# Kernel optimization log

Measured on AMD Instinct MI355X. Metric: run time of the kernel, lower is better.

The kernel has to match this reference:

```python
import jax, jax.numpy as jnp
import numpy as np

TEMPERATURE = 0.05


def setup_inputs() -> dict:
    key = jax.random.key(0)
    k1, k2, k3 = jax.random.split(key, 3)
    B, D = 8192, 256
    return {
        "embedding_anchor": jax.random.normal(k1, (B, D), dtype=jnp.float32),
        "embedding_pos": jax.random.normal(k2, (B, D), dtype=jnp.float32),
        "embedding_neg": jax.random.normal(k3, (B, D), dtype=jnp.float32),
    }


def _l2norm(x, eps=1e-12):
    # torch.nn.functional.normalize: x / max(||x||, eps)
    n = jnp.sqrt(jnp.sum(x * x, axis=1, keepdims=True))
    return x / jnp.maximum(n, eps)


def reference(embedding_anchor, embedding_pos, embedding_neg):
    B = embedding_anchor.shape[0]
    targets = jnp.concatenate([embedding_pos, embedding_neg], axis=0)  # [2B, D]
    a = _l2norm(embedding_anchor)
    t = _l2norm(targets)
    scores = (a @ t.T) / TEMPERATURE  # [B, 2B]
    # Chunked CE with per-chunk weight len(labels)/B == full-batch mean CE
    logp = jax.nn.log_softmax(scores, axis=1)
    labels = jnp.arange(B)
    loss = -jnp.mean(jnp.take_along_axis(logp, labels[:, None], axis=1))
    return loss
```

## Files before the change

kernel.cpp:

```cpp
#include <hip/hip_runtime.h>
#include <hip/hip_bf16.h>

#define D 256
#define TEMP_INV 20.0f
#define NJ 16
#define NS (NJ * 8)

typedef __attribute__((ext_vector_type(8))) short bf16x8s;
typedef __attribute__((ext_vector_type(4))) float f32x4;

__device__ __forceinline__ unsigned short f2bf(float f) {
  unsigned u = __float_as_uint(f);
  unsigned r = u + 0x7FFFu + ((u >> 16) & 1u);
  return (unsigned short)(r >> 16);
}

__device__ __forceinline__ void gld16(const void* g, void* l) {
  __builtin_amdgcn_global_load_lds(
      (const __attribute__((address_space(1))) void*)g,
      (__attribute__((address_space(3))) void*)l, 16, 0, 0);
}

__global__ __launch_bounds__(256) void nce_normalize(const float* __restrict__ anc,
                                                     const float* __restrict__ pos,
                                                     const float* __restrict__ neg,
                                                     unsigned short* __restrict__ An,
                                                     unsigned short* __restrict__ Tn,
                                                     float* __restrict__ rowsum,
                                                     int B) {
  int zi = blockIdx.x * 256 + threadIdx.x;
  if (blockIdx.x < (B + 255) / 256 && zi < B) rowsum[zi] = 0.0f;

  const int lane = threadIdx.x & 63;
  const int wid  = threadIdx.x >> 6;
  const int sub  = lane >> 4, lr = lane & 15;
  int row = blockIdx.x * 16 + wid * 4 + sub;

  const float* src;
  unsigned short* dst;
  int r2;
  if (row < B)          { src = anc; dst = An; r2 = row; }
  else if (row < 2 * B) { src = pos; dst = Tn; r2 = row - B; }
  else                  { src = neg; dst = Tn + (size_t)B * D; r2 = row - 2 * B; }

  const float4* sp = reinterpret_cast<const float4*>(src) + (size_t)r2 * (D / 4);
  float4 v[4];
#pragma unroll
  for (int c = 0; c < 4; ++c) v[c] = sp[lr + c * 16];
  float ss = 0.0f;
#pragma unroll
  for (int c = 0; c < 4; ++c)
    ss += v[c].x * v[c].x + v[c].y * v[c].y + v[c].z * v[c].z + v[c].w * v[c].w;
  ss += __shfl_xor(ss, 1, 64);
  ss += __shfl_xor(ss, 2, 64);
  ss += __shfl_xor(ss, 4, 64);
  ss += __shfl_xor(ss, 8, 64);
  float inv = rsqrtf(fmaxf(ss, 1e-24f));
  ushort4* dp = reinterpret_cast<ushort4*>(dst) + (size_t)r2 * (D / 4);
#pragma unroll
  for (int c = 0; c < 4; ++c) {
    ushort4 o;
    o.x = f2bf(v[c].x * inv);
    o.y = f2bf(v[c].y * inv);
    o.z = f2bf(v[c].z * inv);
    o.w = f2bf(v[c].w * inv);
    dp[lr + c * 16] = o;
  }
}

__global__ __launch_bounds__(256, 2) void nce_scores(const unsigned short* __restrict__ A,
                                                     const unsigned short* __restrict__ T,
                                                     float* __restrict__ rowsum,
                                                     float* __restrict__ diag) {
  __shared__ unsigned char smem[4][8192];

  const int tid  = threadIdx.x;
  const int lane = tid & 63;
  const int wid  = __builtin_amdgcn_readfirstlane(tid >> 6);
  const int wr = wid >> 1, wc = wid & 1;
  const int row0 = blockIdx.y * 128;
  const int cg   = blockIdx.x;
  const int r = lane & 15, g = lane >> 4;

  const int pp    = (lane & 7) ^ (lane >> 3);
  const int Rbase = 2 * (lane >> 3) + (pp >> 2);
  const int Cb    = pp & 3;
  const unsigned char* gB = (const unsigned char*)T +
      (((size_t)(cg * 2048 + wid * 32 + Rbase)) << 9) + Cb * 16;

  auto STAGE = [&](int s) {
    const unsigned char* gb = gB + (size_t)(s >> 3) * 65536 + (s & 7) * 64;
    unsigned char* sb = &smem[s & 3][0];
    gld16(gb,        sb + wid * 2048);
    gld16(gb + 8192, sb + wid * 2048 + 1024);
  };

  const int S7   = (r >> 1) & 7;
  const int pA   = (((r & 1) << 2) + g) ^ S7;
  const int offF = ((r >> 1) << 7) + (pA << 4);
  const int offB = wc * 4096 + offF;

  const unsigned short* aPtr = A + (size_t)(row0 + wr * 64 + r) * D + g * 8;
  bf16x8s aF[4][8];
#pragma unroll
  for (int m = 0; m < 4; ++m)
#pragma unroll
    for (int kt = 0; kt < 8; ++kt)
      aF[m][kt] = *reinterpret_cast<const bf16x8s*>(aPtr + (size_t)m * 16 * D + kt * 32);

  STAGE(0);
  STAGE(1);
  STAGE(2);

  float rs[4][4];
#pragma unroll
  for (int m = 0; m < 4; ++m)
#pragma unroll
    for (int reg = 0; reg < 4; ++reg) rs[m][reg] = 0.0f;

  for (int j = 0; j < NJ; ++j) {
    f32x4 acc[4][4];
#pragma unroll
    for (int m = 0; m < 4; ++m)
#pragma unroll
      for (int n = 0; n < 4; ++n) acc[m][n] = (f32x4)0.0f;

#pragma unroll
    for (int kt = 0; kt < 8; ++kt) {
      const int s = j * 8 + kt;
      asm volatile("s_waitcnt vmcnt(4)" ::: "memory");
      __builtin_amdgcn_s_barrier();
      const unsigned char* sb = &smem[s & 3][0];
      bf16x8s bF[4];
#pragma unroll
      for (int n = 0; n < 4; ++n)
        bF[n] = *reinterpret_cast<const bf16x8s*>(sb + offB + n * 1024);
      if (s + 3 < NS) STAGE(s + 3);
      asm volatile("s_waitcnt lgkmcnt(0)" ::: "memory");
      __builtin_amdgcn_sched_barrier(0);
      __builtin_amdgcn_s_setprio(1);
#pragma unroll
      for (int m = 0; m < 4; ++m)
#pragma unroll
        for (int n = 0; n < 4; ++n)
          acc[m][n] = __builtin_amdgcn_mfma_f32_16x16x32_bf16(aF[m][kt], bF[n], acc[m][n], 0, 0, 0);
      __builtin_amdgcn_s_setprio(0);
      __builtin_amdgcn_sched_barrier(0);
    }

    const bool diagTile = (cg * NJ + j == (int)blockIdx.y);
#pragma unroll
    for (int m = 0; m < 4; ++m) {
#pragma unroll
      for (int reg = 0; reg < 4; ++reg) {
        float s = 0.0f;
#pragma unroll
        for (int n = 0; n < 4; ++n) s += __expf(acc[m][n][reg] * TEMP_INV);
        rs[m][reg] += s;
        if (diagTile && wr == wc && r == g * 4 + reg)
          diag[row0 + wr * 64 + m * 16 + r] = acc[m][m][reg];
      }
    }
  }

#pragma unroll
  for (int m = 0; m < 4; ++m) {
#pragma unroll
    for (int reg = 0; reg < 4; ++reg) {
      float s = rs[m][reg];
      s += __shfl_xor(s, 1, 64);
      s += __shfl_xor(s, 2, 64);
      s += __shfl_xor(s, 4, 64);
      s += __shfl_xor(s, 8, 64);
      if (r == 0) atomicAdd(&rowsum[row0 + wr * 64 + m * 16 + g * 4 + reg], s);
    }
  }
}

__global__ __launch_bounds__(1024) void nce_finalize(const float* __restrict__ rowsum,
                                                     const float* __restrict__ diag,
                                                     float* __restrict__ out, int n) {
  __shared__ float red[16];
  float s = 0.0f;
  for (int i = threadIdx.x; i < n; i += 1024)
    s += logf(rowsum[i]) - diag[i] * TEMP_INV;
#pragma unroll
  for (int m = 1; m < 64; m <<= 1) s += __shfl_xor(s, m, 64);
  if ((threadIdx.x & 63) == 0) red[threadIdx.x >> 6] = s;
  __syncthreads();
  if (threadIdx.x == 0) {
    float t = 0.0f;
#pragma unroll
    for (int i = 0; i < 16; ++i) t += red[i];
    out[0] = t / (float)n;
  }
}

extern "C" void kernel_launch(void* const* d_in, const int* in_sizes, int n_in,
                              void* d_out, int out_size, void* d_ws, size_t ws_size,
                              hipStream_t stream) {
  const float* anc = (const float*)d_in[0];
  const float* pos = (const float*)d_in[1];
  const float* neg = (const float*)d_in[2];
  const int B  = in_sizes[0] / D;
  const int N2 = 2 * B;

  char* ws = (char*)d_ws;
  unsigned short* An = (unsigned short*)ws;
  unsigned short* Tn = (unsigned short*)(ws + (size_t)B * D * 2);
  float* rowsum = (float*)(ws + (size_t)B * D * 2 + (size_t)N2 * D * 2);
  float* diag   = rowsum + B;

  nce_normalize<<<3 * B / 16, 256, 0, stream>>>(anc, pos, neg, An, Tn, rowsum, B);

  dim3 grid(N2 / (NJ * 128), B / 128);
  nce_scores<<<grid, 256, 0, stream>>>(An, Tn, rowsum, diag);

  nce_finalize<<<1, 1024, 0, stream>>>(rowsum, diag, (float*)d_out, B);
}
```

Baseline: 140.1 us.

## Switch scores GEMM to 32x32x16 MFMA with double-buffered LDS fragment prefetch

Replaces the 16x16x32 bf16 MFMA tiling with 32x32x16 MFMAs, so each wave computes 2x2 tiles of 32x32 and needs fewer LDS fragment loads per FLOP. B fragments for the next k-step are prefetched into a register double buffer while the current MFMAs issue, and the LDS swizzle and staging layout are reworked to match. It also halves NJ, which doubles the grid's column blocks, and raises launch bounds to 4 blocks per CU for more parallelism. In exchange it costs more atomics on rowsum, puts more register pressure on the larger accumulators, and adds risk in the new diagonal and row-index mapping.

New measurement: 298.0 us. +112.8%, slower.

```diff
diff --git a/kernel.cpp b/kernel.cpp
--- a/kernel.cpp
+++ b/kernel.cpp
@@ -3,11 +3,11 @@
 
 #define D 256
 #define TEMP_INV 20.0f
-#define NJ 16
+#define NJ 8
 #define NS (NJ * 8)
 
 typedef __attribute__((ext_vector_type(8))) short bf16x8s;
-typedef __attribute__((ext_vector_type(4))) float f32x4;
+typedef __attribute__((ext_vector_type(16))) float f32x16;
 
 __device__ __forceinline__ unsigned short f2bf(float f) {
   unsigned u = __float_as_uint(f);
@@ -68,7 +68,7 @@
   }
 }
 
-__global__ __launch_bounds__(256, 2) void nce_scores(const unsigned short* __restrict__ A,
+__global__ __launch_bounds__(256, 4) void nce_scores(const unsigned short* __restrict__ A,
                                                      const unsigned short* __restrict__ T,
                                                      float* __restrict__ rowsum,
                                                      float* __restrict__ diag) {
@@ -80,101 +80,131 @@
   const int wr = wid >> 1, wc = wid & 1;
   const int row0 = blockIdx.y * 128;
   const int cg   = blockIdx.x;
-  const int r = lane & 15, g = lane >> 4;
-
-  const int pp    = (lane & 7) ^ (lane >> 3);
-  const int Rbase = 2 * (lane >> 3) + (pp >> 2);
-  const int Cb    = pp & 3;
+  const int r32 = lane & 31, g2 = lane >> 5;
+
+  const int Rl = lane >> 2;
+  const int Cl = (lane & 3) ^ ((lane >> 3) & 3);
   const unsigned char* gB = (const unsigned char*)T +
-      (((size_t)(cg * 2048 + wid * 32 + Rbase)) << 9) + Cb * 16;
-
-  auto STAGE = [&](int s) {
-    const unsigned char* gb = gB + (size_t)(s >> 3) * 65536 + (s & 7) * 64;
-    unsigned char* sb = &smem[s & 3][0];
+      (((size_t)(cg * 1024 + wid * 32 + Rl)) << 9) + Cl * 16;
+
+  auto STAGE = [&](int j2, int kt2, int buf) {
+    const unsigned char* gb = gB + (size_t)j2 * 65536 + kt2 * 64;
+    unsigned char* sb = &smem[buf][0];
     gld16(gb,        sb + wid * 2048);
     gld16(gb + 8192, sb + wid * 2048 + 1024);
   };
 
-  const int S7   = (r >> 1) & 7;
-  const int pA   = (((r & 1) << 2) + g) ^ S7;
-  const int offF = ((r >> 1) << 7) + (pA << 4);
-  const int offB = wc * 4096 + offF;
-
-  const unsigned short* aPtr = A + (size_t)(row0 + wr * 64 + r) * D + g * 8;
-  bf16x8s aF[4][8];
-#pragma unroll
-  for (int m = 0; m < 4; ++m)
-#pragma unroll
-    for (int kt = 0; kt < 8; ++kt)
-      aF[m][kt] = *reinterpret_cast<const bf16x8s*>(aPtr + (size_t)m * 16 * D + kt * 32);
-
-  STAGE(0);
-  STAGE(1);
-  STAGE(2);
-
-  float rs[4][4];
-#pragma unroll
-  for (int m = 0; m < 4; ++m)
-#pragma unroll
-    for (int reg = 0; reg < 4; ++reg) rs[m][reg] = 0.0f;
+  const int xr = (r32 >> 1) & 3;
+  int offB[2][2];
+#pragma unroll
+  for (int s2 = 0; s2 < 2; ++s2)
+#pragma unroll
+    for (int n = 0; n < 2; ++n)
+      offB[s2][n] = ((wc * 64 + n * 32 + r32) << 6) + ((((s2 << 1) | g2) ^ xr) << 4);
+
+  const unsigned short* aPtr = A + (size_t)(row0 + wr * 64 + r32) * D + g2 * 8;
+  bf16x8s aF[2][16];
+#pragma unroll
+  for (int m = 0; m < 2; ++m)
+#pragma unroll
+    for (int ks = 0; ks < 16; ++ks)
+      aF[m][ks] = *reinterpret_cast<const bf16x8s*>(aPtr + (size_t)m * 32 * D + ks * 16);
+
+  float rs[2][16];
+#pragma unroll
+  for (int m = 0; m < 2; ++m)
+#pragma unroll
+    for (int reg = 0; reg < 16; ++reg) rs[m][reg] = 0.0f;
+
+  bf16x8s bF[2][2][2];
+
+  STAGE(0, 0, 0);
+  STAGE(0, 1, 1);
+  STAGE(0, 2, 2);
+  asm volatile("s_waitcnt vmcnt(4)" ::: "memory");
+  __builtin_amdgcn_s_barrier();
+  {
+    const unsigned char* sb0 = &smem[0][0];
+#pragma unroll
+    for (int s2 = 0; s2 < 2; ++s2)
+#pragma unroll
+      for (int n = 0; n < 2; ++n)
+        bF[0][s2][n] = *reinterpret_cast<const bf16x8s*>(sb0 + offB[s2][n]);
+  }
 
   for (int j = 0; j < NJ; ++j) {
-    f32x4 acc[4][4];
-#pragma unroll
-    for (int m = 0; m < 4; ++m)
-#pragma unroll
-      for (int n = 0; n < 4; ++n) acc[m][n] = (f32x4)0.0f;
+    f32x16 acc[2][2];
+#pragma unroll
+    for (int m = 0; m < 2; ++m)
+#pragma unroll
+      for (int n = 0; n < 2; ++n) acc[m][n] = (f32x16)0.0f;
 
 #pragma unroll
     for (int kt = 0; kt < 8; ++kt) {
-      const int s = j * 8 + kt;
-      asm volatile("s_waitcnt vmcnt(4)" ::: "memory");
+      asm volatile("s_waitcnt vmcnt(2)" ::: "memory");
       __builtin_amdgcn_s_barrier();
-      const unsigned char* sb = &smem[s & 3][0];
-      bf16x8s bF[4];
-#pragma unroll
-      for (int n = 0; n < 4; ++n)
-        bF[n] = *reinterpret_cast<const bf16x8s*>(sb + offB + n * 1024);
-      if (s + 3 < NS) STAGE(s + 3);
-      asm volatile("s_waitcnt lgkmcnt(0)" ::: "memory");
+      {
+        const int j2  = j + ((kt + 3) >> 3);
+        const int kt2 = (kt + 3) & 7;
+        if (j2 < NJ) STAGE(j2, kt2, (kt + 3) & 3);
+      }
+      {
+        const unsigned char* sbn = &smem[(kt + 1) & 3][0];
+#pragma unroll
+        for (int s2 = 0; s2 < 2; ++s2)
+#pragma unroll
+          for (int n = 0; n < 2; ++n)
+            bF[(kt + 1) & 1][s2][n] =
+                *reinterpret_cast<const bf16x8s*>(sbn + offB[s2][n]);
+      }
+      asm volatile("s_waitcnt lgkmcnt(4)" ::: "memory");
       __builtin_amdgcn_sched_barrier(0);
       __builtin_amdgcn_s_setprio(1);
 #pragma unroll
-      for (int m = 0; m < 4; ++m)
-#pragma unroll
-        for (int n = 0; n < 4; ++n)
-          acc[m][n] = __builtin_amdgcn_mfma_f32_16x16x32_bf16(aF[m][kt], bF[n], acc[m][n], 0, 0, 0);
+      for (int s2 = 0; s2 < 2; ++s2)
+#pragma unroll
+        for (int m = 0; m < 2; ++m)
+#pragma unroll
+          for (int n = 0; n < 2; ++n)
+            acc[m][n] = __builtin_amdgcn_mfma_f32_32x32x16_bf16(
+                aF[m][kt * 2 + s2], bF[kt & 1][s2][n], acc[m][n], 0, 0, 0);
       __builtin_amdgcn_s_setprio(0);
       __builtin_amdgcn_sched_barrier(0);
     }
 
-    const bool diagTile = (cg * NJ + j == (int)blockIdx.y);
-#pragma unroll
-    for (int m = 0; m < 4; ++m) {
-#pragma unroll
-      for (int reg = 0; reg < 4; ++reg) {
-        float s = 0.0f;
-#pragma unroll
-        for (int n = 0; n < 4; ++n) s += __expf(acc[m][n][reg] * TEMP_INV);
-        rs[m][reg] += s;
-        if (diagTile && wr == wc && r == g * 4 + reg)
-          diag[row0 + wr * 64 + m * 16 + r] = acc[m][m][reg];
-      }
+#pragma unroll
+    for (int m = 0; m < 2; ++m)
+#pragma unroll
+      for (int reg = 0; reg < 16; ++reg)
+        rs[m][reg] += __expf(acc[m][0][reg] * TEMP_INV) +
+                      __expf(acc[m][1][reg] * TEMP_INV);
+
+    const bool diagT = (cg * NJ + j == (int)blockIdx.y);
+    if (diagT && wr == wc) {
+#pragma unroll
+      for (int m = 0; m < 2; ++m)
+#pragma unroll
+        for (int reg = 0; reg < 16; ++reg) {
+          const int crow = (reg & 3) + 8 * (reg >> 2) + 4 * g2;
+          if (r32 == crow)
+            diag[row0 + wr * 64 + m * 32 + crow] = acc[m][m][reg];
+        }
     }
   }
 
 #pragma unroll
-  for (int m = 0; m < 4; ++m) {
-#pragma unroll
-    for (int reg = 0; reg < 4; ++reg) {
+  for (int m = 0; m < 2; ++m)
+#pragma unroll
+    for (int reg = 0; reg < 16; ++reg) {
       float s = rs[m][reg];
       s += __shfl_xor(s, 1, 64);
       s += __shfl_xor(s, 2, 64);
       s += __shfl_xor(s, 4, 64);
       s += __shfl_xor(s, 8, 64);
-      if (r == 0) atomicAdd(&rowsum[row0 + wr * 64 + m * 16 + g * 4 + reg], s);
+      s += __shfl_xor(s, 16, 64);
+      if (r32 == 0)
+        atomicAdd(&rowsum[row0 + wr * 64 + m * 32 + (reg & 3) + 8 * (reg >> 2) + 4 * g2], s);
     }
-  }
 }
 
 __global__ __launch_bounds__(1024) void nce_finalize(const float* __restrict__ rowsum,
```

## Double-buffer LDS B-fragment reads and fuse finalize into scores via last-block counter

Applied to the files above, without the earlier changes.

Prefetches the next k-step's B fragments from LDS into a second register buffer while MFMAs run on the current one, relaxing the vmcnt/lgkmcnt waits. It also removes the separate finalize kernel: each scores block increments a global counter, and the last block computes the log-sum reduction and writes the loss. This cuts LDS-read latency stalls and one kernel launch, at the cost of more registers and a serial tail in one block.

After: 192.3 us. 37.3% more time.

```diff
diff --git a/kernel.cpp b/kernel.cpp
--- a/kernel.cpp
+++ b/kernel.cpp
@@ -27,9 +27,11 @@
                                                      unsigned short* __restrict__ An,
                                                      unsigned short* __restrict__ Tn,
                                                      float* __restrict__ rowsum,
+                                                     int* __restrict__ counter,
                                                      int B) {
   int zi = blockIdx.x * 256 + threadIdx.x;
   if (blockIdx.x < (B + 255) / 256 && zi < B) rowsum[zi] = 0.0f;
+  if (blockIdx.x == 0 && threadIdx.x == 0) *counter = 0;
 
   const int lane = threadIdx.x & 63;
   const int wid  = threadIdx.x >> 6;
@@ -71,8 +73,13 @@
 __global__ __launch_bounds__(256, 2) void nce_scores(const unsigned short* __restrict__ A,
                                                      const unsigned short* __restrict__ T,
                                                      float* __restrict__ rowsum,
-                                                     float* __restrict__ diag) {
+                                                     float* __restrict__ diag,
+                                                     int* __restrict__ counter,
+                                                     float* __restrict__ out,
+                                                     int B, int nblocks) {
   __shared__ unsigned char smem[4][8192];
+  __shared__ float red[4];
+  __shared__ int lastFlag;
 
   const int tid  = threadIdx.x;
   const int lane = tid & 63;
@@ -118,6 +125,17 @@
 #pragma unroll
     for (int reg = 0; reg < 4; ++reg) rs[m][reg] = 0.0f;
 
+  bf16x8s bF[2][4];
+
+  asm volatile("s_waitcnt vmcnt(4)" ::: "memory");
+  __builtin_amdgcn_s_barrier();
+  {
+    const unsigned char* sb0 = &smem[0][0];
+#pragma unroll
+    for (int n = 0; n < 4; ++n)
+      bF[0][n] = *reinterpret_cast<const bf16x8s*>(sb0 + offB + n * 1024);
+  }
+
   for (int j = 0; j < NJ; ++j) {
     f32x4 acc[4][4];
 #pragma unroll
@@ -128,22 +146,24 @@
 #pragma unroll
     for (int kt = 0; kt < 8; ++kt) {
       const int s = j * 8 + kt;
-      asm volatile("s_waitcnt vmcnt(4)" ::: "memory");
+      asm volatile("s_waitcnt vmcnt(2)" ::: "memory");
       __builtin_amdgcn_s_barrier();
-      const unsigned char* sb = &smem[s & 3][0];
-      bf16x8s bF[4];
-#pragma unroll
-      for (int n = 0; n < 4; ++n)
-        bF[n] = *reinterpret_cast<const bf16x8s*>(sb + offB + n * 1024);
       if (s + 3 < NS) STAGE(s + 3);
-      asm volatile("s_waitcnt lgkmcnt(0)" ::: "memory");
+      {
+        const unsigned char* sbn = &smem[(kt + 1) & 3][0];
+#pragma unroll
+        for (int n = 0; n < 4; ++n)
+          bF[(kt + 1) & 1][n] =
+              *reinterpret_cast<const bf16x8s*>(sbn + offB + n * 1024);
+      }
+      asm volatile("s_waitcnt lgkmcnt(4)" ::: "memory");
       __builtin_amdgcn_sched_barrier(0);
       __builtin_amdgcn_s_setprio(1);
 #pragma unroll
       for (int m = 0; m < 4; ++m)
 #pragma unroll
         for (int n = 0; n < 4; ++n)
-          acc[m][n] = __builtin_amdgcn_mfma_f32_16x16x32_bf16(aF[m][kt], bF[n], acc[m][n], 0, 0, 0);
+          acc[m][n] = __builtin_amdgcn_mfma_f32_16x16x32_bf16(aF[m][kt], bF[kt & 1][n], acc[m][n], 0, 0, 0);
       __builtin_amdgcn_s_setprio(0);
       __builtin_amdgcn_sched_barrier(0);
     }
@@ -175,24 +195,20 @@
       if (r == 0) atomicAdd(&rowsum[row0 + wr * 64 + m * 16 + g * 4 + reg], s);
     }
   }
-}
-
-__global__ __launch_bounds__(1024) void nce_finalize(const float* __restrict__ rowsum,
-                                                     const float* __restrict__ diag,
-                                                     float* __restrict__ out, int n) {
-  __shared__ float red[16];
-  float s = 0.0f;
-  for (int i = threadIdx.x; i < n; i += 1024)
-    s += logf(rowsum[i]) - diag[i] * TEMP_INV;
-#pragma unroll
-  for (int m = 1; m < 64; m <<= 1) s += __shfl_xor(s, m, 64);
-  if ((threadIdx.x & 63) == 0) red[threadIdx.x >> 6] = s;
+
+  __threadfence();
+  if (tid == 0) lastFlag = (atomicAdd(counter, 1) == nblocks - 1);
   __syncthreads();
-  if (threadIdx.x == 0) {
-    float t = 0.0f;
-#pragma unroll
-    for (int i = 0; i < 16; ++i) t += red[i];
-    out[0] = t / (float)n;
+  if (lastFlag) {
+    __threadfence();
+    float s = 0.0f;
+    for (int i = tid; i < B; i += 256)
+      s += logf(rowsum[i]) - diag[i] * TEMP_INV;
+#pragma unroll
+    for (int m = 1; m < 64; m <<= 1) s += __shfl_xor(s, m, 64);
+    if ((tid & 63) == 0) red[tid >> 6] = s;
+    __syncthreads();
+    if (tid == 0) out[0] = (red[0] + red[1] + red[2] + red[3]) / (float)B;
   }
 }
 
@@ -210,11 +226,11 @@
   unsigned short* Tn = (unsigned short*)(ws + (size_t)B * D * 2);
   float* rowsum = (float*)(ws + (size_t)B * D * 2 + (size_t)N2 * D * 2);
   float* diag   = rowsum + B;
-
-  nce_normalize<<<3 * B / 16, 256, 0, stream>>>(anc, pos, neg, An, Tn, rowsum, B);
+  int* counter  = (int*)(diag + B);
+
+  nce_normalize<<<3 * B / 16, 256, 0, stream>>>(anc, pos, neg, An, Tn, rowsum, counter, B);
 
   dim3 grid(N2 / (NJ * 128), B / 128);
-  nce_scores<<<grid, 256, 0, stream>>>(An, Tn, rowsum, diag);
-
-  nce_finalize<<<1, 1024, 0, stream>>>(rowsum, diag, (float*)d_out, B);
-}
+  nce_scores<<<grid, 256, 0, stream>>>(An, Tn, rowsum, diag, counter,
+                                       (float*)d_out, B, grid.x * grid.y);
+}
```

## Double K-step per pipeline stage and use raw exp2 in softmax sum

Applied to the files above, without the earlier changes.

Each pipeline stage now loads a 64-wide K slice (16KB per buffer) instead of 32, halving the number of barriers and waits per tile and issuing 32 MFMAs per barrier. The LDS swizzle and load layout are redone for 128-byte rows, with B-fragment offsets precomputed. The exponential uses the hardware exp2 with a folded constant, which avoids the scaling inside __expf. LDS usage doubles to 64KB per block, which may limit occupancy with launch bounds of 2 blocks per CU.

New measurement: 139.2 us. About the same (-0.6%).

```diff
diff --git a/kernel.cpp b/kernel.cpp
--- a/kernel.cpp
+++ b/kernel.cpp
@@ -3,8 +3,9 @@
 
 #define D 256
 #define TEMP_INV 20.0f
+#define K_EXP2 28.85390081777927f
 #define NJ 16
-#define NS (NJ * 8)
+#define NS (NJ * 4)
 
 typedef __attribute__((ext_vector_type(8))) short bf16x8s;
 typedef __attribute__((ext_vector_type(4))) float f32x4;
@@ -72,7 +73,7 @@
                                                      const unsigned short* __restrict__ T,
                                                      float* __restrict__ rowsum,
                                                      float* __restrict__ diag) {
-  __shared__ unsigned char smem[4][8192];
+  __shared__ unsigned char smem[4][16384];
 
   const int tid  = threadIdx.x;
   const int lane = tid & 63;
@@ -82,31 +83,35 @@
   const int cg   = blockIdx.x;
   const int r = lane & 15, g = lane >> 4;
 
-  const int pp    = (lane & 7) ^ (lane >> 3);
-  const int Rbase = 2 * (lane >> 3) + (pp >> 2);
-  const int Cb    = pp & 3;
+  const int Rl = lane >> 3;
+  const int Cl = (lane & 7) ^ Rl;
   const unsigned char* gB = (const unsigned char*)T +
-      (((size_t)(cg * 2048 + wid * 32 + Rbase)) << 9) + Cb * 16;
+      (((size_t)(cg * 2048 + wid * 32 + Rl)) << 9) + Cl * 16;
 
   auto STAGE = [&](int s) {
-    const unsigned char* gb = gB + (size_t)(s >> 3) * 65536 + (s & 7) * 64;
+    const unsigned char* gb = gB + (size_t)(s >> 2) * 65536 + (s & 3) * 128;
     unsigned char* sb = &smem[s & 3][0];
-    gld16(gb,        sb + wid * 2048);
-    gld16(gb + 8192, sb + wid * 2048 + 1024);
+#pragma unroll
+    for (int q = 0; q < 4; ++q)
+      gld16(gb + q * 4096, sb + wid * 4096 + q * 1024);
   };
 
-  const int S7   = (r >> 1) & 7;
-  const int pA   = (((r & 1) << 2) + g) ^ S7;
-  const int offF = ((r >> 1) << 7) + (pA << 4);
-  const int offB = wc * 4096 + offF;
+  const int rx = r & 7;
+  int offB[2][4];
+#pragma unroll
+  for (int ks = 0; ks < 2; ++ks)
+#pragma unroll
+    for (int n = 0; n < 4; ++n)
+      offB[ks][n] = wc * 8192 + n * 2048 + r * 128 + ((((ks << 2) | g) ^ rx) << 4);
 
   const unsigned short* aPtr = A + (size_t)(row0 + wr * 64 + r) * D + g * 8;
   bf16x8s aF[4][8];
 #pragma unroll
   for (int m = 0; m < 4; ++m)
 #pragma unroll
-    for (int kt = 0; kt < 8; ++kt)
-      aF[m][kt] = *reinterpret_cast<const bf16x8s*>(aPtr + (size_t)m * 16 * D + kt * 32);
+    for (int t = 0; t < 8; ++t)
+      aF[m][t] = *reinterpret_cast<const bf16x8s*>(aPtr + (size_t)m * 16 * D + t * 32);
+  __builtin_amdgcn_sched_barrier(0);
 
   STAGE(0);
   STAGE(1);
@@ -126,24 +131,29 @@
       for (int n = 0; n < 4; ++n) acc[m][n] = (f32x4)0.0f;
 
 #pragma unroll
-    for (int kt = 0; kt < 8; ++kt) {
-      const int s = j * 8 + kt;
-      asm volatile("s_waitcnt vmcnt(4)" ::: "memory");
+    for (int kt = 0; kt < 4; ++kt) {
+      const int s = j * 4 + kt;
+      asm volatile("s_waitcnt vmcnt(8)" ::: "memory");
       __builtin_amdgcn_s_barrier();
-      const unsigned char* sb = &smem[s & 3][0];
-      bf16x8s bF[4];
-#pragma unroll
-      for (int n = 0; n < 4; ++n)
-        bF[n] = *reinterpret_cast<const bf16x8s*>(sb + offB + n * 1024);
+      const unsigned char* sb = &smem[kt][0];
+      bf16x8s bF[2][4];
+#pragma unroll
+      for (int ks = 0; ks < 2; ++ks)
+#pragma unroll
+        for (int n = 0; n < 4; ++n)
+          bF[ks][n] = *reinterpret_cast<const bf16x8s*>(sb + offB[ks][n]);
       if (s + 3 < NS) STAGE(s + 3);
       asm volatile("s_waitcnt lgkmcnt(0)" ::: "memory");
       __builtin_amdgcn_sched_barrier(0);
       __builtin_amdgcn_s_setprio(1);
 #pragma unroll
-      for (int m = 0; m < 4; ++m)
-#pragma unroll
-        for (int n = 0; n < 4; ++n)
-          acc[m][n] = __builtin_amdgcn_mfma_f32_16x16x32_bf16(aF[m][kt], bF[n], acc[m][n], 0, 0, 0);
+      for (int ks = 0; ks < 2; ++ks)
+#pragma unroll
+        for (int m = 0; m < 4; ++m)
+#pragma unroll
+          for (int n = 0; n < 4; ++n)
+            acc[m][n] = __builtin_amdgcn_mfma_f32_16x16x32_bf16(
+                aF[m][kt * 2 + ks], bF[ks][n], acc[m][n], 0, 0, 0);
       __builtin_amdgcn_s_setprio(0);
       __builtin_amdgcn_sched_barrier(0);
     }
@@ -155,7 +165,8 @@
       for (int reg = 0; reg < 4; ++reg) {
         float s = 0.0f;
 #pragma unroll
-        for (int n = 0; n < 4; ++n) s += __expf(acc[m][n][reg] * TEMP_INV);
+        for (int n = 0; n < 4; ++n)
+          s += __builtin_amdgcn_exp2f(acc[m][n][reg] * K_EXP2);
         rs[m][reg] += s;
         if (diagTile && wr == wc && r == g * 4 + reg)
           diag[row0 + wr * 64 + m * 16 + r] = acc[m][m][reg];
```
